# Optimization experiments

Hardware: AMD Instinct MI355X
Metric: run time of the kernel (lower is better)

## Reference

```python
import jax, jax.numpy as jnp
import numpy as np

WINDOW = (1, 7, 7)
DIM_HEAD = 32


def _rel_pos_index(ws):
    d, h, w = ws
    coords = np.stack(np.meshgrid(np.arange(d), np.arange(h), np.arange(w), indexing='ij'))
    cf = coords.reshape(3, -1)                      # [3, N]
    rel = (cf[:, :, None] - cf[:, None, :]).transpose(1, 2, 0).copy()  # [N, N, 3]
    rel[..., 0] += d - 1
    rel[..., 1] += h - 1
    rel[..., 2] += w - 1
    rel[..., 0] *= (2 * h - 1) * (2 * w - 1)
    rel[..., 1] *= (2 * w - 1)
    return jnp.asarray(rel.sum(-1))                 # [N, N] int32, N = 49


REL_IDX = _rel_pos_index(WINDOW)


def setup_inputs() -> dict:
    key = jax.random.key(0)
    k1, k2, k3, k4, k5 = jax.random.split(key, 5)
    B, X, Y, W1, W2, D = 4, 32, 32, 7, 7, 512
    heads = D // DIM_HEAD
    n_bias = (2 * WINDOW[0] - 1) * (2 * WINDOW[1] - 1) * (2 * WINDOW[2] - 1)  # 169
    s = 1.0 / np.sqrt(D)
    return {
        'x': jax.random.normal(k1, (B, X, Y, W1, W2, D), jnp.float32),
        'y': jax.random.normal(k2, (B, X, Y, W1, W2, D), jnp.float32),
        'Wq': jax.random.normal(k3, (D, D), jnp.float32) * s,
        'Wkv': jax.random.normal(k4, (D, 2 * D), jnp.float32) * s,
        'bias_table': jax.random.normal(k5, (n_bias, heads), jnp.float32) * 0.02,
    }


def reference(x, y, Wq, Wkv, bias_table):
    B, X, Y, W1, W2, D = x.shape
    h = D // DIM_HEAD
    n = W1 * W2                                     # 49 tokens per window
    scale = DIM_HEAD ** -0.5

    xr = x.reshape(B * X * Y, n, D)                 # [Bw, n, D]
    yr = y.reshape(B * X * Y, n, D)

    q = xr @ Wq                                     # [Bw, n, D]
    kv = yr @ Wkv                                   # [Bw, n, 2D]
    k, v = kv[..., :D], kv[..., D:]

    def to_heads(t):
        return t.reshape(t.shape[0], n, h, DIM_HEAD).transpose(0, 2, 1, 3)  # [Bw, h, n, dh]

    q, k, v = to_heads(q), to_heads(k), to_heads(v)

    sim = jnp.einsum('bhid,bhjd->bhij', q, k) * scale   # [Bw, h, n, n]
    bias = bias_table[REL_IDX]                          # [n, n, h]
    sim = sim + bias.transpose(2, 0, 1)[None]           # broadcast over windows

    attn = jax.nn.softmax(sim, axis=-1)
    out = jnp.einsum('bhij,bhjd->bhid', attn, v)        # [Bw, h, n, dh]
    out = out.transpose(0, 2, 1, 3).reshape(B * X * Y, W1, W2, D)
    return out.reshape(B, X, Y, W1, W2, D)
```

## Files before the change

### kernel.cpp

```cpp
#include <hip/hip_runtime.h>


typedef __bf16 bf16x8 __attribute__((ext_vector_type(8)));
typedef __attribute__((ext_vector_type(4))) float f32x4;

#define DEVI __device__ __forceinline__

DEVI unsigned short f2bf(float f) {
  union { float f; unsigned u; } v; v.f = f;
  unsigned r = v.u + 0x7FFFu + ((v.u >> 16) & 1u);
  return (unsigned short)(r >> 16);
}
DEVI unsigned pkbf(float a, float b) {
  return (unsigned)f2bf(a) | ((unsigned)f2bf(b) << 16);
}

#define MFMA16(a, b, c) __builtin_amdgcn_mfma_f32_16x16x32_bf16((a), (b), (c), 0, 0, 0)

#define SWZ_Y(r)  ((((unsigned)(r)) & 7u) << 4)
#define SWZ_A(r)  (((((unsigned)(r)) >> 2) & 3u) << 5)
#define SWZ_P(r)  ((((unsigned)(r)) & 7u) << 4)
#define SWZ_VT(r) ((((unsigned)(r)) & 7u) << 4)

__global__ void prep_kernel(const float* __restrict__ Wq, const float* __restrict__ Wkv,
                            const float* __restrict__ bt, char* __restrict__ ws) {
  int t = blockIdx.x * 256 + threadIdx.x;
  if (t < 786432) {
    int e = t & 7, lane = (t >> 3) & 63, ks = (t >> 9) & 15, nt = (t >> 13) & 1,
        h = (t >> 14) & 15, T = t >> 18;
    int row = ks * 32 + (lane >> 4) * 8 + e;
    int col = h * 32 + nt * 16 + (lane & 15);
    float v;
    if (T == 0)      v = Wq[row * 512 + col] * 0.17677669529663687f;
    else if (T == 1) v = Wkv[row * 1024 + col];
    else             v = Wkv[row * 1024 + 512 + col];
    ((unsigned short*)ws)[t] = f2bf(v);
  }
  if (t < 262144) {
    int r = t & 3, lane = (t >> 2) & 63, jt = (t >> 8) & 3, it = (t >> 10) & 3,
        h = (t >> 12) & 15;
    int i = it * 16 + (lane & 15);
    int j = jt * 16 + ((lane >> 4) & 3) * 4 + r;
    float v;
    if (j >= 49)      v = -1e30f;
    else if (i >= 49) v = 0.0f;
    else {
      int hi = i / 7, wi = i % 7, hj = j / 7, wj = j % 7;
      v = bt[((hi - hj + 6) * 13 + (wi - wj + 6)) * 16 + h];
    }
    ((float*)(ws + 1572864))[t] = v;
  }
}

DEVI bf16x8 ldXY(const char* base, int row, int kc) {
  unsigned a = ((unsigned)(row * 1024 + kc * 2)) ^ SWZ_Y(row);
  return *(const bf16x8*)(base + a);
}
DEVI bf16x8 ldXY_c(const char* base, int row, int kc) {
  int rc = row < 48 ? row : 48;
  bf16x8 v = ldXY(base, rc, kc);
  if (row > 48) {
    union { long long z[2]; bf16x8 v; } u; u.z[0] = 0; u.z[1] = 0;
    v = u.v;
  }
  return v;
}
DEVI bf16x8 ldQK(const char* base, int row, int kc) {
  int rc = row < 48 ? row : 48;
  unsigned a = ((unsigned)(rc * 64 + kc * 2)) ^ SWZ_A(rc);
  return *(const bf16x8*)(base + a);
}
DEVI bf16x8 ldP2(const char* base, int row, int jc) {
  int rc = row < 48 ? row : 48;
  unsigned a = ((unsigned)(rc * 128 + jc * 2)) ^ SWZ_P(rc);
  return *(const bf16x8*)(base + a);
}
DEVI bf16x8 ldVT(const char* base, int dh, int jc) {
  unsigned a = ((unsigned)(dh * 128 + jc * 2)) ^ SWZ_VT(dh);
  return *(const bf16x8*)(base + a);
}

__global__ __launch_bounds__(1024, 4)
void attn_kernel(const float* __restrict__ x, const float* __restrict__ y,
                 const char* __restrict__ wsW, const float* __restrict__ biasD,
                 float* __restrict__ out) {
  extern __shared__ char smem[];
  char* xb = smem;
  char* yb = smem + 50176;
  const int tid = threadIdx.x;
  const int lane = tid & 63, wave = tid >> 6;
  const int quad = wave >> 2, m2 = (wave >> 1) & 1, n2 = wave & 1, iw = wave & 3;
  const int g = lane >> 4, lr = lane & 15;
  char* pbase = smem + 100352 + quad * 10368;
  char* qb = pbase;
  char* kb = pbase + 3136;
  char* vt = pbase + 6272;
  char* Pb = pbase;

  const int bw = blockIdx.x;
  const float* xs = x + (size_t)bw * 25088;
  const float* ys = y + (size_t)bw * 25088;

  for (int it = tid; it < 6272; it += 1024) {
    float4 v = ((const float4*)xs)[it];
    float4 w = ((const float4*)ys)[it];
    int i = it >> 7;
    int k = (it & 127) << 2;
    unsigned a = ((unsigned)(i * 1024 + k * 2)) ^ SWZ_Y(i);
    uint2 ux, uy;
    ux.x = pkbf(v.x, v.y); ux.y = pkbf(v.z, v.w);
    uy.x = pkbf(w.x, w.y); uy.y = pkbf(w.z, w.w);
    *(uint2*)(xb + a) = ux;
    *(uint2*)(yb + a) = uy;
  }

  const bf16x8* wsQ = (const bf16x8*)wsW;
  const bf16x8* wsK = (const bf16x8*)(wsW + 524288);
  const bf16x8* wsV = (const bf16x8*)(wsW + 1048576);
  const f32x4* bD = (const f32x4*)biasD;
  const f32x4 fz = {0.f, 0.f, 0.f, 0.f};

  const int r0 = m2 * 32 + lr;
  const int r1 = m2 * 32 + 16 + lr;

  for (int hi = 0; hi < 4; ++hi) {
    const int h = quad * 4 + hi;

    __syncthreads();

    f32x4 accq[2];
    accq[0] = fz; accq[1] = fz;
    {
      const bf16x8* pQ = wsQ + (size_t)((h * 2 + n2) * 16) * 64 + lane;
      bf16x8 qsr[8];
      #pragma unroll
      for (int i = 0; i < 8; ++i) qsr[i] = pQ[i * 64];
      #pragma unroll
      for (int ks = 0; ks < 16; ++ks) {
        bf16x8 bq = qsr[ks & 7];
        if (ks < 8) qsr[ks & 7] = pQ[(ks + 8) * 64];
        int kc = ks * 32 + g * 8;
        bf16x8 a0 = ldXY(xb, r0, kc);
        bf16x8 a1 = ldXY_c(xb, r1, kc);
        accq[0] = MFMA16(a0, bq, accq[0]);
        accq[1] = MFMA16(a1, bq, accq[1]);
      }
    }
    #pragma unroll
    for (int mt = 0; mt < 2; ++mt)
      #pragma unroll
      for (int r = 0; r < 4; ++r) {
        int row = m2 * 32 + mt * 16 + g * 4 + r;
        if (row < 49) {
          unsigned a = ((unsigned)(row * 64 + (n2 * 16 + lr) * 2)) ^ SWZ_A(row);
          *(unsigned short*)(qb + a) = f2bf(accq[mt][r]);
        }
      }

    f32x4 acck[2], accv[2];
    acck[0] = fz; acck[1] = fz; accv[0] = fz; accv[1] = fz;
    {
      const bf16x8* pK = wsK + (size_t)((h * 2 + n2) * 16) * 64 + lane;
      const bf16x8* pV = wsV + (size_t)((h * 2 + n2) * 16) * 64 + lane;
      bf16x8 ksr[8], vsr[8];
      #pragma unroll
      for (int i = 0; i < 8; ++i) { ksr[i] = pK[i * 64]; vsr[i] = pV[i * 64]; }
      #pragma unroll
      for (int ks = 0; ks < 16; ++ks) {
        bf16x8 bk = ksr[ks & 7], bv = vsr[ks & 7];
        if (ks < 8) {
          ksr[ks & 7] = pK[(ks + 8) * 64];
          vsr[ks & 7] = pV[(ks + 8) * 64];
        }
        int kc = ks * 32 + g * 8;
        bf16x8 a0 = ldXY(yb, r0, kc);
        bf16x8 a1 = ldXY_c(yb, r1, kc);
        acck[0] = MFMA16(a0, bk, acck[0]);
        acck[1] = MFMA16(a1, bk, acck[1]);
        accv[0] = MFMA16(a0, bv, accv[0]);
        accv[1] = MFMA16(a1, bv, accv[1]);
      }
    }
    #pragma unroll
    for (int mt = 0; mt < 2; ++mt) {
      #pragma unroll
      for (int r = 0; r < 4; ++r) {
        int row = m2 * 32 + mt * 16 + g * 4 + r;
        if (row < 49) {
          unsigned a = ((unsigned)(row * 64 + (n2 * 16 + lr) * 2)) ^ SWZ_A(row);
          *(unsigned short*)(kb + a) = f2bf(acck[mt][r]);
        }
      }
      int dh = n2 * 16 + lr;
      int t0 = m2 * 32 + mt * 16 + g * 4;
      unsigned a = ((unsigned)(dh * 128 + t0 * 2)) ^ SWZ_VT(dh);
      uint2 pk;
      pk.x = pkbf(accv[mt][0], accv[mt][1]);
      pk.y = pkbf(accv[mt][2], accv[mt][3]);
      *(uint2*)(vt + a) = pk;
    }

    __syncthreads();

    f32x4 bias[4];
    #pragma unroll
    for (int jt = 0; jt < 4; ++jt)
      bias[jt] = bD[(size_t)(((h * 4 + iw) * 4 + jt) * 64 + lane)];

    bf16x8 qa = ldQK(qb, iw * 16 + lr, g * 8);
    bf16x8 kf[4];
    #pragma unroll
    for (int jt = 0; jt < 4; ++jt) kf[jt] = ldQK(kb, jt * 16 + lr, g * 8);

    f32x4 vals[4];
    #pragma unroll
    for (int jt = 0; jt < 4; ++jt) vals[jt] = MFMA16(kf[jt], qa, fz);
    #pragma unroll
    for (int jt = 0; jt < 4; ++jt) vals[jt] = vals[jt] + bias[jt];

    uint2 pks[4];
    {
      float m = vals[0][0];
      #pragma unroll
      for (int jt = 0; jt < 4; ++jt)
        #pragma unroll
        for (int r = 0; r < 4; ++r) m = fmaxf(m, vals[jt][r]);
      m = fmaxf(m, __shfl_xor(m, 16));
      m = fmaxf(m, __shfl_xor(m, 32));
      float s = 0.f;
      #pragma unroll
      for (int jt = 0; jt < 4; ++jt)
        #pragma unroll
        for (int r = 0; r < 4; ++r) {
          float pv = __expf(vals[jt][r] - m);
          vals[jt][r] = pv;
          s += pv;
        }
      s += __shfl_xor(s, 16);
      s += __shfl_xor(s, 32);
      float inv = 1.0f / s;
      #pragma unroll
      for (int jt = 0; jt < 4; ++jt) {
        pks[jt].x = pkbf(vals[jt][0] * inv, vals[jt][1] * inv);
        pks[jt].y = pkbf(vals[jt][2] * inv, vals[jt][3] * inv);
      }
    }

    __syncthreads();

    {
      int i = iw * 16 + lr;
      if (i < 49) {
        #pragma unroll
        for (int jt = 0; jt < 4; ++jt) {
          unsigned a = ((unsigned)(i * 128 + (jt * 16 + g * 4) * 2)) ^ SWZ_P(i);
          *(uint2*)(Pb + a) = pks[jt];
        }
      }
    }

    f32x4 acco[2];
    acco[0] = fz; acco[1] = fz;
    #pragma unroll
    for (int ks = 0; ks < 2; ++ks) {
      int jc = ks * 32 + g * 8;
      bf16x8 av0 = ldVT(vt, lr, jc);
      bf16x8 av1 = ldVT(vt, lr + 16, jc);
      bf16x8 bp = ldP2(Pb, iw * 16 + lr, jc);
      acco[0] = MFMA16(av0, bp, acco[0]);
      acco[1] = MFMA16(av1, bp, acco[1]);
    }

    float* ow = out + (size_t)bw * 25088 + h * 32;
    {
      int tok = iw * 16 + lr;
      if (tok < 49) {
        #pragma unroll
        for (int md = 0; md < 2; ++md)
          *(f32x4*)(&ow[(size_t)tok * 512 + md * 16 + g * 4]) = acco[md];
      }
    }
  }
}

extern "C" void kernel_launch(void* const* d_in, const int* in_sizes, int n_in,
                              void* d_out, int out_size, void* d_ws, size_t ws_size,
                              hipStream_t stream) {
  (void)in_sizes; (void)n_in; (void)out_size; (void)ws_size;
  const float* x = (const float*)d_in[0];
  const float* y = (const float*)d_in[1];
  const float* Wq = (const float*)d_in[2];
  const float* Wkv = (const float*)d_in[3];
  const float* bt = (const float*)d_in[4];
  float* out = (float*)d_out;
  char* ws = (char*)d_ws;

  prep_kernel<<<3072, 256, 0, stream>>>(Wq, Wkv, bt, ws);

  (void)hipFuncSetAttribute((const void*)attn_kernel,
                            hipFuncAttributeMaxDynamicSharedMemorySize, 141824);
  attn_kernel<<<4096, 1024, 141824, stream>>>(x, y, (const char*)ws,
                                              (const float*)(ws + 1572864), out);
}
```

Before: 851.3 us.

## Switch attention kernel to 32x32x16 MFMA tiles with 512-thread blocks

Replaces the 16x16x32 bf16 MFMA tiling with 32x32x16 MFMAs, so each wave computes a full 32-token by 32-dim tile for the Q/K/V projections, QK^T and PV. The block shrinks from 16 to 8 waves, each pair of waves handling four heads, and the weight and bias prepack layouts are reordered to match the new fragment layout. The aim is fewer MFMA issues and fewer redundant LDS A-fragment loads per output, plus one fewer cross-lane shuffle step in the softmax. In exchange each wave does more serial work per block, and per-thread register pressure rises with the 16-wide accumulators.

```diff
diff --git a/kernel.cpp b/kernel.cpp
--- a/kernel.cpp
+++ b/kernel.cpp
@@ -3,6 +3,7 @@
 
 typedef __bf16 bf16x8 __attribute__((ext_vector_type(8)));
 typedef __attribute__((ext_vector_type(4))) float f32x4;
+typedef __attribute__((ext_vector_type(16))) float f32x16;
 
 #define DEVI __device__ __forceinline__
 
@@ -15,7 +16,7 @@
   return (unsigned)f2bf(a) | ((unsigned)f2bf(b) << 16);
 }
 
-#define MFMA16(a, b, c) __builtin_amdgcn_mfma_f32_16x16x32_bf16((a), (b), (c), 0, 0, 0)
+#define MFMA32(a, b, c) __builtin_amdgcn_mfma_f32_32x32x16_bf16((a), (b), (c), 0, 0, 0)
 
 #define SWZ_Y(r)  ((((unsigned)(r)) & 7u) << 4)
 #define SWZ_A(r)  (((((unsigned)(r)) >> 2) & 3u) << 5)
@@ -26,27 +27,27 @@
                             const float* __restrict__ bt, char* __restrict__ ws) {
   int t = blockIdx.x * 256 + threadIdx.x;
   if (t < 786432) {
-    int e = t & 7, lane = (t >> 3) & 63, ks = (t >> 9) & 15, nt = (t >> 13) & 1,
+    int e = t & 7, lane = (t >> 3) & 63, ks = (t >> 9) & 31,
         h = (t >> 14) & 15, T = t >> 18;
-    int row = ks * 32 + (lane >> 4) * 8 + e;
-    int col = h * 32 + nt * 16 + (lane & 15);
+    int row = ks * 16 + (lane >> 5) * 8 + e;
+    int col = h * 32 + (lane & 31);
     float v;
     if (T == 0)      v = Wq[row * 512 + col] * 0.17677669529663687f;
     else if (T == 1) v = Wkv[row * 1024 + col];
     else             v = Wkv[row * 1024 + 512 + col];
     ((unsigned short*)ws)[t] = f2bf(v);
   }
-  if (t < 262144) {
-    int r = t & 3, lane = (t >> 2) & 63, jt = (t >> 8) & 3, it = (t >> 10) & 3,
+  if (t < 65536) {
+    int reg = t & 15, lane = (t >> 4) & 63, jt = (t >> 10) & 1, it = (t >> 11) & 1,
         h = (t >> 12) & 15;
-    int i = it * 16 + (lane & 15);
-    int j = jt * 16 + ((lane >> 4) & 3) * 4 + r;
+    int i = it * 32 + (lane & 31);
+    int j = jt * 32 + (reg & 3) + 8 * (reg >> 2) + 4 * (lane >> 5);
     float v;
     if (j >= 49)      v = -1e30f;
     else if (i >= 49) v = 0.0f;
     else {
-      int hi = i / 7, wi = i % 7, hj = j / 7, wj = j % 7;
-      v = bt[((hi - hj + 6) * 13 + (wi - wj + 6)) * 16 + h];
+      int hi2 = i / 7, wi = i % 7, hj = j / 7, wj = j % 7;
+      v = bt[((hi2 - hj + 6) * 13 + (wi - wj + 6)) * 16 + h];
     }
     ((float*)(ws + 1572864))[t] = v;
   }
@@ -55,15 +56,6 @@
 DEVI bf16x8 ldXY(const char* base, int row, int kc) {
   unsigned a = ((unsigned)(row * 1024 + kc * 2)) ^ SWZ_Y(row);
   return *(const bf16x8*)(base + a);
-}
-DEVI bf16x8 ldXY_c(const char* base, int row, int kc) {
-  int rc = row < 48 ? row : 48;
-  bf16x8 v = ldXY(base, rc, kc);
-  if (row > 48) {
-    union { long long z[2]; bf16x8 v; } u; u.z[0] = 0; u.z[1] = 0;
-    v = u.v;
-  }
-  return v;
 }
 DEVI bf16x8 ldQK(const char* base, int row, int kc) {
   int rc = row < 48 ? row : 48;
@@ -80,7 +72,7 @@
   return *(const bf16x8*)(base + a);
 }
 
-__global__ __launch_bounds__(1024, 4)
+__global__ __launch_bounds__(512, 2)
 void attn_kernel(const float* __restrict__ x, const float* __restrict__ y,
                  const char* __restrict__ wsW, const float* __restrict__ biasD,
                  float* __restrict__ out) {
@@ -89,9 +81,9 @@
   char* yb = smem + 50176;
   const int tid = threadIdx.x;
   const int lane = tid & 63, wave = tid >> 6;
-  const int quad = wave >> 2, m2 = (wave >> 1) & 1, n2 = wave & 1, iw = wave & 3;
-  const int g = lane >> 4, lr = lane & 15;
-  char* pbase = smem + 100352 + quad * 10368;
+  const int p = wave >> 1, sub = wave & 1;
+  const int il = lane & 31, hi = lane >> 5;
+  char* pbase = smem + 100352 + p * 10368;
   char* qb = pbase;
   char* kb = pbase + 3136;
   char* vt = pbase + 6272;
@@ -101,7 +93,7 @@
   const float* xs = x + (size_t)bw * 25088;
   const float* ys = y + (size_t)bw * 25088;
 
-  for (int it = tid; it < 6272; it += 1024) {
+  for (int it = tid; it < 6272; it += 512) {
     float4 v = ((const float4*)xs)[it];
     float4 w = ((const float4*)ys)[it];
     int i = it >> 7;
@@ -117,167 +109,174 @@
   const bf16x8* wsQ = (const bf16x8*)wsW;
   const bf16x8* wsK = (const bf16x8*)(wsW + 524288);
   const bf16x8* wsV = (const bf16x8*)(wsW + 1048576);
-  const f32x4* bD = (const f32x4*)biasD;
-  const f32x4 fz = {0.f, 0.f, 0.f, 0.f};
-
-  const int r0 = m2 * 32 + lr;
-  const int r1 = m2 * 32 + 16 + lr;
-
-  for (int hi = 0; hi < 4; ++hi) {
-    const int h = quad * 4 + hi;
+  const float* bD = (const float*)biasD;
+  const f32x16 fz16 = {0,0,0,0, 0,0,0,0, 0,0,0,0, 0,0,0,0};
+
+  int arow = sub * 32 + il; if (arow > 48) arow = 48;
+  const int kfb = hi * 8;
+
+  for (int hh = 0; hh < 4; ++hh) {
+    const int h = p * 4 + hh;
 
     __syncthreads();
 
-    f32x4 accq[2];
-    accq[0] = fz; accq[1] = fz;
-    {
-      const bf16x8* pQ = wsQ + (size_t)((h * 2 + n2) * 16) * 64 + lane;
+    f32x16 aq = fz16;
+    {
+      const bf16x8* pQ = wsQ + (size_t)(h * 32) * 64 + lane;
       bf16x8 qsr[8];
       #pragma unroll
       for (int i = 0; i < 8; ++i) qsr[i] = pQ[i * 64];
       #pragma unroll
-      for (int ks = 0; ks < 16; ++ks) {
+      for (int ks = 0; ks < 32; ++ks) {
         bf16x8 bq = qsr[ks & 7];
-        if (ks < 8) qsr[ks & 7] = pQ[(ks + 8) * 64];
-        int kc = ks * 32 + g * 8;
-        bf16x8 a0 = ldXY(xb, r0, kc);
-        bf16x8 a1 = ldXY_c(xb, r1, kc);
-        accq[0] = MFMA16(a0, bq, accq[0]);
-        accq[1] = MFMA16(a1, bq, accq[1]);
-      }
-    }
-    #pragma unroll
-    for (int mt = 0; mt < 2; ++mt)
-      #pragma unroll
-      for (int r = 0; r < 4; ++r) {
-        int row = m2 * 32 + mt * 16 + g * 4 + r;
+        if (ks < 24) qsr[ks & 7] = pQ[(ks + 8) * 64];
+        bf16x8 af = ldXY(xb, arow, ks * 16 + kfb);
+        aq = MFMA32(af, bq, aq);
+      }
+    }
+    #pragma unroll
+    for (int rq = 0; rq < 4; ++rq)
+      #pragma unroll
+      for (int r2 = 0; r2 < 4; ++r2) {
+        int row = sub * 32 + rq * 8 + hi * 4 + r2;
         if (row < 49) {
-          unsigned a = ((unsigned)(row * 64 + (n2 * 16 + lr) * 2)) ^ SWZ_A(row);
-          *(unsigned short*)(qb + a) = f2bf(accq[mt][r]);
-        }
-      }
-
-    f32x4 acck[2], accv[2];
-    acck[0] = fz; acck[1] = fz; accv[0] = fz; accv[1] = fz;
-    {
-      const bf16x8* pK = wsK + (size_t)((h * 2 + n2) * 16) * 64 + lane;
-      const bf16x8* pV = wsV + (size_t)((h * 2 + n2) * 16) * 64 + lane;
+          unsigned a = ((unsigned)(row * 64 + il * 2)) ^ SWZ_A(row);
+          *(unsigned short*)(qb + a) = f2bf(aq[rq * 4 + r2]);
+        }
+      }
+
+    f32x16 ak = fz16, av = fz16;
+    {
+      const bf16x8* pK = wsK + (size_t)(h * 32) * 64 + lane;
+      const bf16x8* pV = wsV + (size_t)(h * 32) * 64 + lane;
       bf16x8 ksr[8], vsr[8];
       #pragma unroll
       for (int i = 0; i < 8; ++i) { ksr[i] = pK[i * 64]; vsr[i] = pV[i * 64]; }
       #pragma unroll
-      for (int ks = 0; ks < 16; ++ks) {
+      for (int ks = 0; ks < 32; ++ks) {
         bf16x8 bk = ksr[ks & 7], bv = vsr[ks & 7];
-        if (ks < 8) {
+        if (ks < 24) {
           ksr[ks & 7] = pK[(ks + 8) * 64];
           vsr[ks & 7] = pV[(ks + 8) * 64];
         }
-        int kc = ks * 32 + g * 8;
-        bf16x8 a0 = ldXY(yb, r0, kc);
-        bf16x8 a1 = ldXY_c(yb, r1, kc);
-        acck[0] = MFMA16(a0, bk, acck[0]);
-        acck[1] = MFMA16(a1, bk, acck[1]);
-        accv[0] = MFMA16(a0, bv, accv[0]);
-        accv[1] = MFMA16(a1, bv, accv[1]);
-      }
-    }
-    #pragma unroll
-    for (int mt = 0; mt < 2; ++mt) {
-      #pragma unroll
-      for (int r = 0; r < 4; ++r) {
-        int row = m2 * 32 + mt * 16 + g * 4 + r;
+        bf16x8 af = ldXY(yb, arow, ks * 16 + kfb);
+        ak = MFMA32(af, bk, ak);
+        av = MFMA32(af, bv, av);
+      }
+    }
+    #pragma unroll
+    for (int rq = 0; rq < 4; ++rq) {
+      #pragma unroll
+      for (int r2 = 0; r2 < 4; ++r2) {
+        int row = sub * 32 + rq * 8 + hi * 4 + r2;
         if (row < 49) {
-          unsigned a = ((unsigned)(row * 64 + (n2 * 16 + lr) * 2)) ^ SWZ_A(row);
-          *(unsigned short*)(kb + a) = f2bf(acck[mt][r]);
-        }
-      }
-      int dh = n2 * 16 + lr;
-      int t0 = m2 * 32 + mt * 16 + g * 4;
-      unsigned a = ((unsigned)(dh * 128 + t0 * 2)) ^ SWZ_VT(dh);
+          unsigned a = ((unsigned)(row * 64 + il * 2)) ^ SWZ_A(row);
+          *(unsigned short*)(kb + a) = f2bf(ak[rq * 4 + r2]);
+        }
+      }
+      int t0 = sub * 32 + rq * 8 + hi * 4;
+      unsigned a = ((unsigned)(il * 128 + t0 * 2)) ^ SWZ_VT(il);
       uint2 pk;
-      pk.x = pkbf(accv[mt][0], accv[mt][1]);
-      pk.y = pkbf(accv[mt][2], accv[mt][3]);
+      pk.x = pkbf(av[rq * 4 + 0], av[rq * 4 + 1]);
+      pk.y = pkbf(av[rq * 4 + 2], av[rq * 4 + 3]);
       *(uint2*)(vt + a) = pk;
     }
 
     __syncthreads();
 
-    f32x4 bias[4];
-    #pragma unroll
-    for (int jt = 0; jt < 4; ++jt)
-      bias[jt] = bD[(size_t)(((h * 4 + iw) * 4 + jt) * 64 + lane)];
-
-    bf16x8 qa = ldQK(qb, iw * 16 + lr, g * 8);
-    bf16x8 kf[4];
-    #pragma unroll
-    for (int jt = 0; jt < 4; ++jt) kf[jt] = ldQK(kb, jt * 16 + lr, g * 8);
-
-    f32x4 vals[4];
-    #pragma unroll
-    for (int jt = 0; jt < 4; ++jt) vals[jt] = MFMA16(kf[jt], qa, fz);
-    #pragma unroll
-    for (int jt = 0; jt < 4; ++jt) vals[jt] = vals[jt] + bias[jt];
-
-    uint2 pks[4];
-    {
+    f32x16 bias[2];
+    #pragma unroll
+    for (int jt = 0; jt < 2; ++jt) {
+      const f32x4* bp = (const f32x4*)(bD + ((size_t)(((h * 2 + sub) * 2 + jt) * 64 + lane)) * 16);
+      #pragma unroll
+      for (int q4 = 0; q4 < 4; ++q4) {
+        f32x4 b4 = bp[q4];
+        bias[jt][q4 * 4 + 0] = b4[0]; bias[jt][q4 * 4 + 1] = b4[1];
+        bias[jt][q4 * 4 + 2] = b4[2]; bias[jt][q4 * 4 + 3] = b4[3];
+      }
+    }
+
+    bf16x8 bq0 = ldQK(qb, sub * 32 + il, kfb);
+    bf16x8 bq1 = ldQK(qb, sub * 32 + il, 16 + kfb);
+    f32x16 sim[2];
+    #pragma unroll
+    for (int jt = 0; jt < 2; ++jt) {
+      bf16x8 ak0 = ldQK(kb, jt * 32 + il, kfb);
+      bf16x8 ak1 = ldQK(kb, jt * 32 + il, 16 + kfb);
+      f32x16 s = MFMA32(ak0, bq0, fz16);
+      sim[jt] = MFMA32(ak1, bq1, s);
+    }
+
+    uint2 pks[2][4];
+    {
+      f32x16 vals[2];
+      #pragma unroll
+      for (int jt = 0; jt < 2; ++jt)
+        #pragma unroll
+        for (int r = 0; r < 16; ++r) vals[jt][r] = sim[jt][r] + bias[jt][r];
       float m = vals[0][0];
       #pragma unroll
-      for (int jt = 0; jt < 4; ++jt)
-        #pragma unroll
-        for (int r = 0; r < 4; ++r) m = fmaxf(m, vals[jt][r]);
-      m = fmaxf(m, __shfl_xor(m, 16));
+      for (int jt = 0; jt < 2; ++jt)
+        #pragma unroll
+        for (int r = 0; r < 16; ++r) m = fmaxf(m, vals[jt][r]);
       m = fmaxf(m, __shfl_xor(m, 32));
       float s = 0.f;
       #pragma unroll
-      for (int jt = 0; jt < 4; ++jt)
-        #pragma unroll
-        for (int r = 0; r < 4; ++r) {
+      for (int jt = 0; jt < 2; ++jt)
+        #pragma unroll
+        for (int r = 0; r < 16; ++r) {
           float pv = __expf(vals[jt][r] - m);
           vals[jt][r] = pv;
           s += pv;
         }
-      s += __shfl_xor(s, 16);
       s += __shfl_xor(s, 32);
       float inv = 1.0f / s;
       #pragma unroll
-      for (int jt = 0; jt < 4; ++jt) {
-        pks[jt].x = pkbf(vals[jt][0] * inv, vals[jt][1] * inv);
-        pks[jt].y = pkbf(vals[jt][2] * inv, vals[jt][3] * inv);
-      }
+      for (int jt = 0; jt < 2; ++jt)
+        #pragma unroll
+        for (int rq = 0; rq < 4; ++rq) {
+          pks[jt][rq].x = pkbf(vals[jt][rq * 4 + 0] * inv, vals[jt][rq * 4 + 1] * inv);
+          pks[jt][rq].y = pkbf(vals[jt][rq * 4 + 2] * inv, vals[jt][rq * 4 + 3] * inv);
+        }
     }
 
     __syncthreads();
 
     {
-      int i = iw * 16 + lr;
+      int i = sub * 32 + il;
       if (i < 49) {
         #pragma unroll
-        for (int jt = 0; jt < 4; ++jt) {
-          unsigned a = ((unsigned)(i * 128 + (jt * 16 + g * 4) * 2)) ^ SWZ_P(i);
-          *(uint2*)(Pb + a) = pks[jt];
-        }
-      }
-    }
-
-    f32x4 acco[2];
-    acco[0] = fz; acco[1] = fz;
-    #pragma unroll
-    for (int ks = 0; ks < 2; ++ks) {
-      int jc = ks * 32 + g * 8;
-      bf16x8 av0 = ldVT(vt, lr, jc);
-      bf16x8 av1 = ldVT(vt, lr + 16, jc);
-      bf16x8 bp = ldP2(Pb, iw * 16 + lr, jc);
-      acco[0] = MFMA16(av0, bp, acco[0]);
-      acco[1] = MFMA16(av1, bp, acco[1]);
+        for (int jt = 0; jt < 2; ++jt)
+          #pragma unroll
+          for (int rq = 0; rq < 4; ++rq) {
+            int j0 = jt * 32 + rq * 8 + hi * 4;
+            unsigned a = ((unsigned)(i * 128 + j0 * 2)) ^ SWZ_P(i);
+            *(uint2*)(Pb + a) = pks[jt][rq];
+          }
+      }
+    }
+
+    f32x16 oacc = fz16;
+    #pragma unroll
+    for (int ks = 0; ks < 4; ++ks) {
+      int jc = ks * 16 + kfb;
+      bf16x8 afv = ldVT(vt, il, jc);
+      bf16x8 bfp = ldP2(Pb, sub * 32 + il, jc);
+      oacc = MFMA32(afv, bfp, oacc);
     }
 
     float* ow = out + (size_t)bw * 25088 + h * 32;
     {
-      int tok = iw * 16 + lr;
+      int tok = sub * 32 + il;
       if (tok < 49) {
         #pragma unroll
-        for (int md = 0; md < 2; ++md)
-          *(f32x4*)(&ow[(size_t)tok * 512 + md * 16 + g * 4]) = acco[md];
+        for (int rq = 0; rq < 4; ++rq) {
+          int dh0 = rq * 8 + hi * 4;
+          f32x4 vv;
+          vv[0] = oacc[rq * 4 + 0]; vv[1] = oacc[rq * 4 + 1];
+          vv[2] = oacc[rq * 4 + 2]; vv[3] = oacc[rq * 4 + 3];
+          *(f32x4*)(&ow[(size_t)tok * 512 + dh0]) = vv;
+        }
       }
     }
   }
@@ -299,6 +298,6 @@
 
   (void)hipFuncSetAttribute((const void*)attn_kernel,
                             hipFuncAttributeMaxDynamicSharedMemorySize, 141824);
-  attn_kernel<<<4096, 1024, 141824, stream>>>(x, y, (const char*)ws,
-                                              (const float*)(ws + 1572864), out);
-}
+  attn_kernel<<<4096, 512, 141824, stream>>>(x, y, (const char*)ws,
+                                             (const float*)(ws + 1572864), out);
+}
```

Result: no change. 848.1 us (-0.4%).
